# Kernel tuning notes

Hardware: AMD Instinct MI355X
Metric: run time of the kernel (lower is better)

Reference implementation:

```python
import jax, jax.numpy as jnp
import numpy as np

B, T, DM, DK, TOPK, NGRAM = 8, 4096, 1024, 256, 4, 3


def setup_inputs() -> dict:
    key = jax.random.key(0)
    k0, k1, k2, k3 = jax.random.split(key, 4)
    std = np.sqrt(2.0 / (DM + DK)).astype(np.float32)
    query = jax.random.normal(k0, (B, T, DM), jnp.float32)
    key_t = jax.random.normal(k1, (B, T, DM), jnp.float32)
    wq = jax.random.normal(k2, (DK, DM), jnp.float32) * std
    wk = jax.random.normal(k3, (DK, DM), jnp.float32) * std
    bq = jnp.zeros((DK,), jnp.float32)
    bk = jnp.zeros((DK,), jnp.float32)
    # Structured mask: each query row keeps exactly TOPK consecutive key columns
    # (required by the module's masked_select -> view(batch, -1, topk)).
    starts = np.minimum(np.arange(T), T - TOPK)
    cols = starts[:, None] + np.arange(TOPK)[None, :]  # [T, TOPK], ascending
    m = np.ones((T, T), dtype=bool)
    m[np.arange(T)[:, None], cols] = False  # False = unmasked
    mask = jnp.asarray(m)[None]  # [1, T, T]
    return {"query": query, "key": key_t, "mask": mask,
            "wq": wq, "bq": bq, "wk": wk, "bk": bk,
            "topk": TOPK, "ngram": NGRAM}


def reference(query, key, mask, wq, bq, wk, bk, topk, ngram):
    # Projections (torch Linear: x @ W.T + b)
    q = jnp.einsum('btm,dm->btd', query, wq) + bq  # [B,T,DK]
    k = jnp.einsum('btm,dm->btd', key, wk) + bk    # [B,T,DK]
    attn = jax.nn.sigmoid(jnp.einsum('btd,bsd->bts', q, k) / 256.0)  # [B,T,T]
    # masked_select of the topk unmasked entries per row, in ascending column
    # order (matches torch row-major masked_select). argsort of bool puts
    # False (unmasked) columns first, stably, i.e. in ascending column order.
    idx = jnp.argsort(mask, axis=-1)[..., :topk]           # [Bm,T,topk]
    idx = jnp.broadcast_to(idx, attn.shape[:2] + (topk,))  # [B,T,topk]
    sp = jnp.take_along_axis(attn, idx, axis=-1)           # [B,T,topk]
    Bsz = sp.shape[0]
    tt = topk * topk
    # init block: [B,topk,topk] -> repeat along new axis -> [B,1,topk,topk*topk]
    sp_init = jnp.tile(sp[:, :topk, :][:, :, None, :], (1, 1, topk, 1)).reshape(Bsz, 1, topk, tt)
    # end block: repeat each element topk times along last axis
    sp_end = jnp.tile(sp[:, -topk:, :][..., None], (1, 1, 1, topk)).reshape(Bsz, 1, topk, tt)
    # middle n-gram blocks
    mid = sp[:, topk:-topk, :].reshape(Bsz, -1, topk, ngram - 1, topk)  # [B,G,topk,2,topk]
    before = mid[:, :, :, 0, :]  # [B,G,topk,topk]
    after = mid[:, :, :, 1, :]   # [B,G,topk,topk]
    sm = jnp.einsum('bgti,bgtj->bgtij', before, after).reshape(Bsz, -1, topk, tt)
    score_matrix = jnp.concatenate([sp_init, sm, sp_end], axis=1)  # [B,G+2,topk,tt]
    return score_matrix.sum(axis=-1)  # [B, G+2, topk]
```

## Files before the change

### kernel.cpp

```cpp
#include <hip/hip_runtime.h>
#include <hip/hip_bf16.h>

#define B_ 8
#define T_ 4096
#define DM_ 1024
#define DK_ 256

typedef __attribute__((ext_vector_type(8))) short short8;
typedef __attribute__((ext_vector_type(4))) float f32x4;
typedef __attribute__((ext_vector_type(4))) unsigned short ushort4v;
typedef __attribute__((ext_vector_type(8))) unsigned short ushort8v;

__device__ inline float bf2f(unsigned short u) {
    union { unsigned int u; float f; } v; v.u = ((unsigned int)u) << 16; return v.f;
}
__device__ inline unsigned short f2bf(float f) {
    __hip_bfloat16 h = __float2bfloat16(f);
    return __builtin_bit_cast(unsigned short, h);
}

__global__ __launch_bounds__(256) void proj_kernel(
    const float* __restrict__ Aq, const float* __restrict__ Ak,
    const float* __restrict__ Wq, const float* __restrict__ Wk,
    const float* __restrict__ bq, const float* __restrict__ bk,
    unsigned short* __restrict__ Oq, unsigned short* __restrict__ Ok)
{
    constexpr int BM = 128, BN = 128, BK = 64;
    __shared__ char smem[(BM + BN) * BK * 2];
    char* As = smem;
    char* Ws = smem + BM * BK * 2;

    const bool isK = (blockIdx.z != 0);
    const float* A    = isK ? Ak : Aq;
    const float* W    = isK ? Wk : Wq;
    const float* bias = isK ? bk : bq;
    unsigned short* O = isK ? Ok : Oq;

    const int row0 = blockIdx.x * BM;
    const int col0 = blockIdx.y * BN;
    const int tid  = threadIdx.x;
    const int lane = tid & 63;
    const int w    = tid >> 6;
    const int wr   = (w >> 1) * 64;
    const int wc   = (w & 1) * 64;
    const int lr   = lane & 15;
    const int lq   = lane >> 4;

    f32x4 acc[4][4];
#pragma unroll
    for (int m = 0; m < 4; ++m)
#pragma unroll
        for (int n = 0; n < 4; ++n) acc[m][n] = (f32x4){0.f, 0.f, 0.f, 0.f};

    const int srow = tid >> 4;
    const int c4   = tid & 15;

    for (int kt = 0; kt < DM_ / BK; ++kt) {
#pragma unroll
        for (int it = 0; it < 8; ++it) {
            int r = srow + it * 16;
            int off = r * 128 + ((c4 * 8) ^ ((r & 7) << 4));
            f32x4 va = *(const f32x4*)(A + (size_t)(row0 + r) * DM_ + kt * BK + c4 * 4);
            ushort4v ua;
#pragma unroll
            for (int e = 0; e < 4; ++e) ua[e] = f2bf(va[e]);
            *(ushort4v*)(As + off) = ua;

            f32x4 vw = *(const f32x4*)(W + (size_t)(col0 + r) * DM_ + kt * BK + c4 * 4);
            ushort4v uw;
#pragma unroll
            for (int e = 0; e < 4; ++e) uw[e] = f2bf(vw[e]);
            *(ushort4v*)(Ws + off) = uw;
        }
        __syncthreads();

#pragma unroll
        for (int kk = 0; kk < 2; ++kk) {
            const int kb = kk * 64 + lq * 16;
            short8 aF[4], bF[4];
#pragma unroll
            for (int m = 0; m < 4; ++m) {
                int r = wr + m * 16 + lr;
                aF[m] = *(const short8*)(As + r * 128 + (kb ^ ((r & 7) << 4)));
            }
#pragma unroll
            for (int n = 0; n < 4; ++n) {
                int r = wc + n * 16 + lr;
                bF[n] = *(const short8*)(Ws + r * 128 + (kb ^ ((r & 7) << 4)));
            }
#pragma unroll
            for (int m = 0; m < 4; ++m)
#pragma unroll
                for (int n = 0; n < 4; ++n)
                    acc[m][n] = __builtin_amdgcn_mfma_f32_16x16x32_bf16(
                        aF[m], bF[n], acc[m][n], 0, 0, 0);
        }
        __syncthreads();
    }

#pragma unroll
    for (int n = 0; n < 4; ++n) {
        int col = col0 + wc + n * 16 + lr;
        float bv = bias[col];
#pragma unroll
        for (int m = 0; m < 4; ++m) {
#pragma unroll
            for (int r = 0; r < 4; ++r) {
                int crow = row0 + wr + m * 16 + lq * 4 + r;
                O[(size_t)crow * DK_ + col] = f2bf(acc[m][n][r] + bv);
            }
        }
    }
}

__global__ __launch_bounds__(256) void score_kernel(
    const unsigned short* __restrict__ Q, const unsigned short* __restrict__ K,
    float* __restrict__ S)
{
    constexpr int RS = 264;
    __shared__ unsigned short qs[64 * RS];
    __shared__ unsigned short ks[68 * RS];

    const int t0  = blockIdx.x * 64;
    const int b   = blockIdx.y;
    const int tid = threadIdx.x;

#pragma unroll
    for (int j = 0; j < 8; ++j) {
        int idx = j * 256 + tid;
        int r = idx >> 5, c = idx & 31;
        ushort8v v = *(const ushort8v*)(Q + ((size_t)(b * T_ + t0 + r)) * DK_ + c * 8);
        *(ushort8v*)(qs + r * RS + c * 8) = v;
    }
#pragma unroll
    for (int j = 0; j < 9; ++j) {
        int idx = j * 256 + tid;
        if (idx < 68 * 32) {
            int r = idx >> 5, c = idx & 31;
            int gr = t0 + r; if (gr > T_ - 1) gr = T_ - 1;
            ushort8v v = *(const ushort8v*)(K + ((size_t)(b * T_ + gr)) * DK_ + c * 8);
            *(ushort8v*)(ks + r * RS + c * 8) = v;
        }
    }
    __syncthreads();

    const int tl = tid >> 2;
    const int i  = tid & 3;
    const int t  = t0 + tl;
    int s = t; if (s > T_ - 4) s = T_ - 4;
    const int kl = s - t0 + i;

    const ushort8v* qr = (const ushort8v*)(qs + tl * RS);
    const ushort8v* kr = (const ushort8v*)(ks + kl * RS);
    float acc = 0.f;
#pragma unroll
    for (int d8 = 0; d8 < 32; ++d8) {
        ushort8v a = qr[d8], bb = kr[d8];
#pragma unroll
        for (int e = 0; e < 8; ++e) acc += bf2f(a[e]) * bf2f(bb[e]);
    }
    float sig = 1.0f / (1.0f + __expf(-acc * (1.0f / 256.0f)));
    sig += __shfl_xor(sig, 1);
    sig += __shfl_xor(sig, 2);
    if (i == 0) S[(size_t)b * T_ + t] = sig;
}

__global__ void out_kernel(const float* __restrict__ S, float* __restrict__ out)
{
    int idx = blockIdx.x * 256 + threadIdx.x;
    if (idx >= B_ * 513 * 4) return;
    int r = idx & 3;
    int g = (idx >> 2) % 513;
    int b = idx / (513 * 4);
    const float* Sb = S + (size_t)b * T_;
    float v;
    if (g == 0)        v = 4.0f * Sb[r];
    else if (g == 512) v = 4.0f * Sb[T_ - 4 + r];
    else { int base = 4 + (g - 1) * 8 + r * 2; v = Sb[base] * Sb[base + 1]; }
    out[idx] = v;
}

extern "C" void kernel_launch(void* const* d_in, const int* in_sizes, int n_in,
                              void* d_out, int out_size, void* d_ws, size_t ws_size,
                              hipStream_t stream)
{
    const float* query = (const float*)d_in[0];
    const float* key   = (const float*)d_in[1];
    const float* wq = (const float*)d_in[3];
    const float* bq = (const float*)d_in[4];
    const float* wk = (const float*)d_in[5];
    const float* bk = (const float*)d_in[6];
    float* out = (float*)d_out;

    unsigned short* Qb = (unsigned short*)d_ws;
    unsigned short* Kb = Qb + (size_t)B_ * T_ * DK_;
    float*          Sb = (float*)(Kb + (size_t)B_ * T_ * DK_);

    dim3 g1(B_ * T_ / 128, DK_ / 128, 2);
    hipLaunchKernelGGL(proj_kernel, g1, dim3(256), 0, stream,
                       query, key, wq, wk, bq, bk, Qb, Kb);

    dim3 g2(T_ / 64, B_);
    hipLaunchKernelGGL(score_kernel, g2, dim3(256), 0, stream, Qb, Kb, Sb);

    int tot = B_ * 513 * 4;
    hipLaunchKernelGGL(out_kernel, dim3((tot + 255) / 256), dim3(256), 0, stream, Sb, out);
}
```

Baseline: 101.8 us.

## Pre-convert weights to bf16 and stream fp32 activations via direct global-to-LDS loads

Adds a small kernel that converts Wq/Wk to bf16 once per call. The projection kernel now covers the full 256-wide output per block with 512 threads, so activations are read only once instead of twice. Tiles are loaded with global_load_lds directly into swizzled LDS, and the fp32 activations are converted to bf16 at fragment-read time. This removes the register round-trip and the duplicated A loads, at the cost of an extra launch, double the LDS footprint for fp32 A, and conversion work in the MFMA inner loop.

```diff
diff --git a/kernel.cpp b/kernel.cpp
--- a/kernel.cpp
+++ b/kernel.cpp
@@ -1,5 +1,6 @@
 #include <hip/hip_runtime.h>
 #include <hip/hip_bf16.h>
+#include <stdint.h>
 
 #define B_ 8
 #define T_ 4096
@@ -19,32 +20,55 @@
     return __builtin_bit_cast(unsigned short, h);
 }
 
-__global__ __launch_bounds__(256) void proj_kernel(
+__device__ inline void gload_lds16(const void* g, void* l) {
+    __builtin_amdgcn_global_load_lds(
+        (const __attribute__((address_space(1))) unsigned int*)g,
+        (__attribute__((address_space(3))) unsigned int*)l, 16, 0, 0);
+}
+
+__global__ __launch_bounds__(256) void convw_kernel(
+    const float* __restrict__ Wq, const float* __restrict__ Wk,
+    unsigned short* __restrict__ Wb)
+{
+    int i = blockIdx.x * 256 + threadIdx.x;
+    const float* src = (i < 65536) ? Wq : Wk;
+    int j = (i < 65536) ? i : i - 65536;
+    f32x4 v = *(const f32x4*)(src + (size_t)j * 4);
+    ushort4v u;
+#pragma unroll
+    for (int e = 0; e < 4; ++e) u[e] = f2bf(v[e]);
+    *(ushort4v*)(Wb + (size_t)i * 4) = u;
+}
+
+__global__ __launch_bounds__(512, 4) void proj_kernel(
     const float* __restrict__ Aq, const float* __restrict__ Ak,
-    const float* __restrict__ Wq, const float* __restrict__ Wk,
+    const unsigned short* __restrict__ Wb,
     const float* __restrict__ bq, const float* __restrict__ bk,
     unsigned short* __restrict__ Oq, unsigned short* __restrict__ Ok)
 {
-    constexpr int BM = 128, BN = 128, BK = 64;
-    __shared__ char smem[(BM + BN) * BK * 2];
+    __shared__ __align__(16) char smem[64 * 1024];
     char* As = smem;
-    char* Ws = smem + BM * BK * 2;
+    char* Ws = smem + 32 * 1024;
 
     const bool isK = (blockIdx.z != 0);
-    const float* A    = isK ? Ak : Aq;
-    const float* W    = isK ? Wk : Wq;
+    const float* A = isK ? Ak : Aq;
+    const unsigned short* W = Wb + (isK ? (size_t)DK_ * DM_ : 0);
     const float* bias = isK ? bk : bq;
     unsigned short* O = isK ? Ok : Oq;
 
-    const int row0 = blockIdx.x * BM;
-    const int col0 = blockIdx.y * BN;
+    const int row0 = blockIdx.x * 128;
     const int tid  = threadIdx.x;
+    const int w    = tid >> 6;
     const int lane = tid & 63;
-    const int w    = tid >> 6;
-    const int wr   = (w >> 1) * 64;
-    const int wc   = (w & 1) * 64;
     const int lr   = lane & 15;
     const int lq   = lane >> 4;
+    const int wr   = (w >> 2) * 64;
+    const int wc   = (w & 3) * 64;
+
+    const int arow  = lane >> 4;
+    const int aslot = lane & 15;
+    const int wrow  = lane >> 3;
+    const int wslot = lane & 7;
 
     f32x4 acc[4][4];
 #pragma unroll
@@ -52,62 +76,60 @@
 #pragma unroll
         for (int n = 0; n < 4; ++n) acc[m][n] = (f32x4){0.f, 0.f, 0.f, 0.f};
 
-    const int srow = tid >> 4;
-    const int c4   = tid & 15;
-
-    for (int kt = 0; kt < DM_ / BK; ++kt) {
-#pragma unroll
-        for (int it = 0; it < 8; ++it) {
-            int r = srow + it * 16;
-            int off = r * 128 + ((c4 * 8) ^ ((r & 7) << 4));
-            f32x4 va = *(const f32x4*)(A + (size_t)(row0 + r) * DM_ + kt * BK + c4 * 4);
-            ushort4v ua;
-#pragma unroll
-            for (int e = 0; e < 4; ++e) ua[e] = f2bf(va[e]);
-            *(ushort4v*)(As + off) = ua;
-
-            f32x4 vw = *(const f32x4*)(W + (size_t)(col0 + r) * DM_ + kt * BK + c4 * 4);
-            ushort4v uw;
-#pragma unroll
-            for (int e = 0; e < 4; ++e) uw[e] = f2bf(vw[e]);
-            *(ushort4v*)(Ws + off) = uw;
+    for (int kt = 0; kt < DM_ / 64; ++kt) {
+        const int kb = kt * 64;
+#pragma unroll
+        for (int i = 0; i < 4; ++i) {
+            const int c = w * 4 + i;
+            const int ra = c * 4 + arow;
+            gload_lds16(A + (size_t)(row0 + ra) * DM_ + kb + ((aslot ^ (ra & 15)) << 2),
+                        As + c * 1024);
+            const int rw = c * 8 + wrow;
+            gload_lds16(W + (size_t)rw * DM_ + kb + ((wslot ^ (rw & 7)) << 3),
+                        Ws + c * 1024);
         }
         __syncthreads();
 
 #pragma unroll
         for (int kk = 0; kk < 2; ++kk) {
-            const int kb = kk * 64 + lq * 16;
-            short8 aF[4], bF[4];
+            short8 bF[4];
+#pragma unroll
+            for (int n = 0; n < 4; ++n) {
+                const int r = wc + n * 16 + lr;
+                const int s = ((kk << 2) + lq) ^ (lr & 7);
+                bF[n] = *(const short8*)(Ws + r * 128 + (s << 4));
+            }
 #pragma unroll
             for (int m = 0; m < 4; ++m) {
-                int r = wr + m * 16 + lr;
-                aF[m] = *(const short8*)(As + r * 128 + (kb ^ ((r & 7) << 4)));
-            }
-#pragma unroll
-            for (int n = 0; n < 4; ++n) {
-                int r = wc + n * 16 + lr;
-                bF[n] = *(const short8*)(Ws + r * 128 + (kb ^ ((r & 7) << 4)));
-            }
-#pragma unroll
-            for (int m = 0; m < 4; ++m)
+                const int r  = wr + m * 16 + lr;
+                const int sb = (kk << 3) + (lq << 1);
+                f32x4 a0 = *(const f32x4*)(As + r * 256 + (((sb)     ^ lr) << 4));
+                f32x4 a1 = *(const f32x4*)(As + r * 256 + (((sb + 1) ^ lr) << 4));
+                short8 aF;
+#pragma unroll
+                for (int e = 0; e < 4; ++e) {
+                    aF[e]     = (short)f2bf(a0[e]);
+                    aF[e + 4] = (short)f2bf(a1[e]);
+                }
 #pragma unroll
                 for (int n = 0; n < 4; ++n)
                     acc[m][n] = __builtin_amdgcn_mfma_f32_16x16x32_bf16(
-                        aF[m], bF[n], acc[m][n], 0, 0, 0);
+                        aF, bF[n], acc[m][n], 0, 0, 0);
+            }
         }
         __syncthreads();
     }
 
 #pragma unroll
     for (int n = 0; n < 4; ++n) {
-        int col = col0 + wc + n * 16 + lr;
-        float bv = bias[col];
+        const int col = wc + n * 16 + lr;
+        const float bv = bias[col];
 #pragma unroll
         for (int m = 0; m < 4; ++m) {
 #pragma unroll
-            for (int r = 0; r < 4; ++r) {
-                int crow = row0 + wr + m * 16 + lq * 4 + r;
-                O[(size_t)crow * DK_ + col] = f2bf(acc[m][n][r] + bv);
+            for (int r4 = 0; r4 < 4; ++r4) {
+                const int crow = row0 + wr + m * 16 + lq * 4 + r4;
+                O[(size_t)crow * DK_ + col] = f2bf(acc[m][n][r4] + bv);
             }
         }
     }
@@ -195,10 +217,13 @@
     unsigned short* Qb = (unsigned short*)d_ws;
     unsigned short* Kb = Qb + (size_t)B_ * T_ * DK_;
     float*          Sb = (float*)(Kb + (size_t)B_ * T_ * DK_);
-
-    dim3 g1(B_ * T_ / 128, DK_ / 128, 2);
-    hipLaunchKernelGGL(proj_kernel, g1, dim3(256), 0, stream,
-                       query, key, wq, wk, bq, bk, Qb, Kb);
+    unsigned short* Wb = (unsigned short*)(Sb + (size_t)B_ * T_);
+
+    hipLaunchKernelGGL(convw_kernel, dim3(512), dim3(256), 0, stream, wq, wk, Wb);
+
+    dim3 g1(B_ * T_ / 128, 1, 2);
+    hipLaunchKernelGGL(proj_kernel, g1, dim3(512), 0, stream,
+                       query, key, Wb, bq, bk, Qb, Kb);
 
     dim3 g2(T_ / 64, B_);
     hipLaunchKernelGGL(score_kernel, g2, dim3(256), 0, stream, Qb, Kb, Sb);
```

After: 82.10 us. -19.4%, faster.
